# Performance work log

Measured on AMD Instinct MI355X. Metric: run time of the kernel, lower is better.

## Reference

```python
import jax, jax.numpy as jnp
import numpy as np

N = 20000
F_IN = 500
HID = 64
CLS = 16
H = 4
K_KNN = 10
NEG_SLOPE = 0.2


def _edges(key, n_rand):
    # random edges plus self-loops (mirrors add_self_loops in the torch code)
    src = jax.random.randint(key, (n_rand,), 0, N)
    dst = jax.random.randint(jax.random.fold_in(key, 1), (n_rand,), 0, N)
    loops = jnp.arange(N)
    return jnp.stack([jnp.concatenate([src, loops]), jnp.concatenate([dst, loops])]).astype(jnp.int32)


def setup_inputs():
    key = jax.random.key(0)
    ks = jax.random.split(key, 40)
    inp = {}
    inp['x'] = jax.random.normal(ks[0], (N, F_IN), jnp.float32)
    inp['edge_index_1'] = _edges(ks[1], 16 * N)          # 1-hop graph, 340k edges
    inp['edge_index_2'] = _edges(ks[2], 32 * N)          # denser 2-hop graph, 660k edges
    knn_src = jnp.repeat(jnp.arange(N), K_KNN)
    knn_dst = jax.random.randint(ks[3], (K_KNN * N,), 0, N)
    inp['edge_index_knn'] = jnp.stack([knn_src, knn_dst]).astype(jnp.int32)

    def p(k, shape):
        return jax.random.normal(k, shape, jnp.float32) * 0.05

    dims = {1: (F_IN, HID), 2: (HID, CLS), 3: (F_IN, HID), 4: (HID, CLS), 5: (F_IN, HID), 6: (HID, CLS)}
    i = 4
    for j in range(1, 7):
        fi, fo = dims[j]
        inp[f'W{j}'] = p(ks[i], (fi, H, fo)); i += 1
        inp[f'as{j}'] = p(ks[i], (H, fo)); i += 1
        inp[f'ad{j}'] = p(ks[i], (H, fo)); i += 1
        inp[f'b{j}'] = jnp.zeros((fo,), jnp.float32)
    for j in range(1, 4):
        inp[f'lin{j}_w'] = p(ks[i], (CLS, CLS)); i += 1
        inp[f'lin{j}_b'] = jnp.zeros((CLS,), jnp.float32)
    inp['agg_w'] = p(ks[i], (CLS,))
    return inp


def gat_conv(x, ei, W, a_s, a_d, b):
    # PyG GATConv, concat=False (mean over heads). W: [F,H,D], a_s/a_d: [H,D], b: [D]
    src, dst = ei[0], ei[1]
    z = jnp.einsum('nf,fhd->nhd', x, W)                 # [N,H,D]
    e_src = jnp.sum(z * a_s, -1)                         # [N,H]
    e_dst = jnp.sum(z * a_d, -1)                         # [N,H]
    e = jax.nn.leaky_relu(e_src[src] + e_dst[dst], NEG_SLOPE)   # [E,H]
    m = jax.ops.segment_max(e, dst, num_segments=N)      # per-dst softmax (edge softmax)
    p = jnp.exp(e - m[dst])
    s = jax.ops.segment_sum(p, dst, num_segments=N)
    alpha = p / (s[dst] + 1e-16)                         # [E,H]
    out = jax.ops.segment_sum(alpha[:, :, None] * z[src], dst, num_segments=N)  # [N,H,D]
    return out.mean(1) + b


def reference(x, edge_index_1, edge_index_2, edge_index_knn,
              W1, as1, ad1, b1, W2, as2, ad2, b2,
              W3, as3, ad3, b3, W4, as4, ad4, b4,
              W5, as5, ad5, b5, W6, as6, ad6, b6,
              lin1_w, lin1_b, lin2_w, lin2_b, lin3_w, lin3_b, agg_w):
    # eval mode: dropout is a no-op
    h1 = jax.nn.relu(gat_conv(x, edge_index_1, W1, as1, ad1, b1))
    h1 = gat_conv(h1, edge_index_1, W2, as2, ad2, b2)
    h2 = jax.nn.relu(gat_conv(x, edge_index_2, W3, as3, ad3, b3))
    h2 = gat_conv(h2, edge_index_2, W4, as4, ad4, b4)
    h3 = jax.nn.relu(gat_conv(x, edge_index_knn, W5, as5, ad5, b5))
    h3 = gat_conv(h3, edge_index_knn, W6, as6, ad6, b6)

    a1 = jnp.tanh(h1 @ lin1_w + lin1_b) @ agg_w          # [N]
    a2 = jnp.tanh(h2 @ lin2_w + lin2_b) @ agg_w
    a3 = jnp.tanh(h3 @ lin3_w + lin3_b) @ agg_w
    a = jax.nn.softmax(jnp.stack([a1, a2, a3], axis=1), axis=1)  # [N,3]
    h = a[:, 0:1] * h1 + a[:, 1:2] * h2 + a[:, 2:3] * h3
    return jax.nn.log_softmax(h, axis=1)
```

## Files before the change

### kernel.cpp

```cpp
#include <hip/hip_runtime.h>
#include <hip/hip_bf16.h>
#include <math.h>

#define N_NODES 20000
#define MP      20096
#define FIN     500
#define KP      512
#define NBUCK   157

typedef unsigned short u16;
typedef unsigned char  u8;
typedef __attribute__((ext_vector_type(8))) short   short8;
typedef __attribute__((ext_vector_type(2))) unsigned uv2;
typedef __attribute__((ext_vector_type(4))) unsigned uv4;
typedef __attribute__((ext_vector_type(2))) float   f32x2;
typedef __attribute__((ext_vector_type(4))) float   f32x4;

__device__ __forceinline__ float b2f(u16 u){
  union { unsigned int i; float f; } v; v.i = ((unsigned int)u) << 16; return v.f;
}
__device__ __forceinline__ u16 f2b(float f){
  __hip_bfloat16 h = __float2bfloat16(f);
  return *reinterpret_cast<u16*>(&h);
}
__device__ __forceinline__ float lrelu(float x){ return x >= 0.f ? x : 0.2f * x; }
__device__ __forceinline__ float ldp(const void* p, int i, int bf){
  return bf ? b2f(((const u16*)p)[i]) : ((const float*)p)[i];
}
__device__ __forceinline__ u8 f2fp8(float f){
  return (u8)(__builtin_amdgcn_cvt_pk_fp8_f32(f, 0.f, 0, false) & 0xff);
}
template<bool HI>
__device__ __forceinline__ f32x2 fp8pair(unsigned w){
  return __builtin_amdgcn_cvt_pk_f32_fp8((int)w, HI);
}
__device__ __forceinline__ void gll16(const u16* g, u16* l){
  __builtin_amdgcn_global_load_lds(
      (const __attribute__((address_space(1))) unsigned int*)g,
      (__attribute__((address_space(3))) unsigned int*)l, 16, 0, 0);
}
__device__ __forceinline__ void barrier_lgkm(){
  asm volatile("s_waitcnt lgkmcnt(0)" ::: "memory");
  __builtin_amdgcn_s_barrier();
  asm volatile("" ::: "memory");
}
__device__ __forceinline__ float ftanh(float x){
  float ex = __expf(2.f * x);
  return 1.f - 2.f / (ex + 1.f);
}

__global__ __launch_bounds__(1024) void detect_dtype_kernel(const unsigned int* __restrict__ xw, int nwords,
                                                            int* __restrict__ flag){
  __shared__ int cnt;
  if (threadIdx.x == 0) cnt = 0;
  __syncthreads();
  int c = 0;
  for (int i = threadIdx.x; i < nwords; i += 1024){
    unsigned e = (xw[i] >> 7) & 0xFF;
    if (e >= 0x70 && e <= 0x8F) c++;
  }
  atomicAdd(&cnt, c);
  __syncthreads();
  if (threadIdx.x == 0) *flag = (cnt * 2 > nwords) ? 1 : 0;
}

#define CHA 8192
#define PB  1024
__global__ __launch_bounds__(PB) void prep_kernel(
    const void* __restrict__ x, u16* __restrict__ xp,
    const void* Wb0, const void* Wb1, const void* Wb2,
    const void* Ws0, const void* Ws1, const void* Ws2,
    u16* ob0, u16* ob1, u16* ob2, u16* os0, u16* os1, u16* os2,
    const int* s0, const int* s1, const int* s2,
    const int* d0, const int* d1, const int* d2,
    int E0, int E1, int E2, int S0, int S1, int S2, int EB,
    int* __restrict__ bucketCur, unsigned* p0, unsigned* p1, unsigned* p2,
    const int* __restrict__ flag){
  __shared__ int hb[NBUCK];
  __shared__ int loff[NBUCK];
  __shared__ int hbase[NBUCK];
  __shared__ unsigned shp[CHA];
  __shared__ u8 shb[CHA];
  __shared__ u16 tile[64][65];
  int bf = *flag;
  int tid = threadIdx.x;
  if (blockIdx.y == 0){
    int t = blockIdx.x * PB + tid;
    if (t >= MP * 64) return;
    int row = t >> 6;
    int j0  = (t & 63) * 8;
    short8 v = {0,0,0,0,0,0,0,0};
    if (row < N_NODES){
      if (j0 + 8 <= FIN){
        if (bf){
          const ushort4* xr = (const ushort4*)((const u16*)x + (size_t)row * FIN + j0);
          ushort4 a = xr[0], b = xr[1];
          v[0]=(short)a.x; v[1]=(short)a.y; v[2]=(short)a.z; v[3]=(short)a.w;
          v[4]=(short)b.x; v[5]=(short)b.y; v[6]=(short)b.z; v[7]=(short)b.w;
        } else {
          const float4* xr = (const float4*)((const float*)x + (size_t)row * FIN + j0);
          float4 a = xr[0], b = xr[1];
          v[0]=(short)f2b(a.x); v[1]=(short)f2b(a.y); v[2]=(short)f2b(a.z); v[3]=(short)f2b(a.w);
          v[4]=(short)f2b(b.x); v[5]=(short)f2b(b.y); v[6]=(short)f2b(b.z); v[7]=(short)f2b(b.w);
        }
      } else {
#pragma unroll
        for (int j = 0; j < 8; ++j){
          int k = j0 + j;
          u16 val = 0;
          if (k < FIN)
            val = bf ? ((const u16*)x)[(size_t)row * FIN + k]
                     : f2b(((const float*)x)[(size_t)row * FIN + k]);
          v[j] = (short)val;
        }
      }
    }
    *(short8*)(xp + (size_t)row * KP + j0) = v;
  } else if (blockIdx.y == 1){
    int xb = blockIdx.x;
    if (xb >= 96 + 3) return;
    int tx = tid & 63, tyb = tid >> 6;
    const void* Wsrc; u16* O; int SRCW, SRCH, DSTW, kt, nt;
    if (xb < 96){
      int which = xb >> 5, tl = xb & 31;
      nt = (tl & 3) << 6; kt = (tl >> 2) << 6;
      Wsrc = which == 0 ? Wb0 : (which == 1 ? Wb1 : Wb2);
      O    = which == 0 ? ob0 : (which == 1 ? ob1 : ob2);
      SRCW = 256; SRCH = FIN; DSTW = KP;
    } else {
      int which = xb - 96;
      nt = 0; kt = 0;
      Wsrc = which == 0 ? Ws0 : (which == 1 ? Ws1 : Ws2);
      O    = which == 0 ? os0 : (which == 1 ? os1 : os2);
      SRCW = 64; SRCH = 64; DSTW = 64;
    }
#pragma unroll
    for (int r = 0; r < 4; ++r){
      int kl = tyb + r * 16;
      int k = kt + kl, n = nt + tx;
      u16 vv = 0;
      if (k < SRCH)
        vv = bf ? ((const u16*)Wsrc)[(size_t)k * SRCW + n]
                : f2b(((const float*)Wsrc)[(size_t)k * SRCW + n]);
      tile[kl][tx] = vv;
    }
    __syncthreads();
#pragma unroll
    for (int r = 0; r < 4; ++r){
      int nl = tyb + r * 16;
      O[(size_t)(nt + nl) * DSTW + kt + tx] = tile[tx][nl];
    }
  } else {
    int sblk = blockIdx.x;
    if (sblk >= 3 * EB) return;
    int g = sblk / EB;
    const int* src = g == 0 ? s0 : (g == 1 ? s1 : s2);
    const int* dst = g == 0 ? d0 : (g == 1 ? d1 : d2);
    unsigned* pairs = g == 0 ? p0 : (g == 1 ? p1 : p2);
    int E = g == 0 ? E0 : (g == 1 ? E1 : E2);
    int S = g == 0 ? S0 : (g == 1 ? S1 : S2);
    int base = (sblk % EB) * CHA;
    if (base >= E) return;
    if (tid < NBUCK) hb[tid] = 0;
    __syncthreads();
    constexpr int EPT = CHA / PB;
    int rk[EPT]; unsigned pr[EPT]; int bk[EPT]; bool vl[EPT];
#pragma unroll
    for (int i = 0; i < EPT; ++i){
      int e = base + i * PB + tid;
      vl[i] = e < E;
      bk[i] = 0; rk[i] = 0; pr[i] = 0;
      if (vl[i]){
        int dd = dst[e], ss = src[e];
        bk[i] = dd >> 7;
        pr[i] = ((unsigned)ss << 7) | (unsigned)(dd & 127);
        rk[i] = atomicAdd(&hb[bk[i]], 1);
      }
    }
    __syncthreads();
    int ret = 0;
    if (tid < NBUCK) ret = atomicAdd(&bucketCur[g * NBUCK + tid], hb[tid]);
    if (tid == 0){
      int run = 0;
      for (int k = 0; k < NBUCK; ++k){ loff[k] = run; run += hb[k]; }
    }
    barrier_lgkm();
#pragma unroll
    for (int i = 0; i < EPT; ++i)
      if (vl[i]){
        int j = loff[bk[i]] + rk[i];
        shp[j] = pr[i];
        shb[j] = (u8)bk[i];
      }
    if (tid < NBUCK) hbase[tid] = ret;
    __syncthreads();
    int nb = E - base; if (nb > CHA) nb = CHA;
    for (int j = tid; j < nb; j += PB){
      int b = shb[j];
      int pos = hbase[b] + (j - loff[b]);
      if (pos < S)
        pairs[(size_t)b * S + pos] = shp[j];
    }
  }
}

__global__ __launch_bounds__(1024) void csr_finalize_kernel(
    const unsigned* p0, const unsigned* p1, const unsigned* p2,
    int S0, int S1, int S2,
    const int* __restrict__ bucketCur,
    int* e0, int* e1, int* e2,
    int2* __restrict__ metaB){
  int g = blockIdx.y;
  const unsigned* pairs = g == 0 ? p0 : (g == 1 ? p1 : p2);
  int* esrc = g == 0 ? e0 : (g == 1 ? e1 : e2);
  int S = g == 0 ? S0 : (g == 1 ? S1 : S2);
  int2* meta = metaB + (size_t)g * MP;
  int b = blockIdx.x;
  int nb = bucketCur[g * NBUCK + b];
  if (nb > S) nb = S;
  const unsigned* pb = pairs + (size_t)b * S;
  int* eb = esrc + (size_t)b * S;
  __shared__ int cnt[128];
  __shared__ int loff[128];
  __shared__ int cur[128];
  if (threadIdx.x < 128) cnt[threadIdx.x] = 0;
  __syncthreads();
  for (int i = threadIdx.x; i < nb; i += 1024)
    atomicAdd(&cnt[pb[i] & 127], 1);
  __syncthreads();
  if (threadIdx.x == 0){
    int run = 0;
    for (int k = 0; k < 128; ++k){ loff[k] = run; run += cnt[k]; }
  }
  __syncthreads();
  if (threadIdx.x < 128){
    cur[threadIdx.x] = loff[threadIdx.x];
    int d = b * 128 + threadIdx.x;
    if (d < N_NODES){
      int2 m; m.x = b * S + loff[threadIdx.x]; m.y = cnt[threadIdx.x];
      meta[d] = m;
    }
  }
  __syncthreads();
  for (int i = threadIdx.x; i < nb; i += 1024){
    unsigned u = pb[i];
    int slot = atomicAdd(&cur[u & 127], 1);
    eb[slot] = (int)(u >> 7);
  }
}

__global__ __launch_bounds__(256) void gemm_big_kernel(const u16* __restrict__ A,
    const u16* B0, const u16* B1, const u16* B2,
    u8* C0, u8* C1, u8* C2,
    const void* as0, const void* as1, const void* as2,
    const void* ad0, const void* ad1, const void* ad2,
    float* __restrict__ esB, float* __restrict__ edB,
    const int* __restrict__ flag, int M){
  int g = blockIdx.z;
  const u16* BT = g == 0 ? B0 : (g == 1 ? B1 : B2);
  u8* C = g == 0 ? C0 : (g == 1 ? C1 : C2);
  const void* as_ = g == 0 ? as0 : (g == 1 ? as1 : as2);
  const void* ad_ = g == 0 ? ad0 : (g == 1 ? ad1 : ad2);
  float* es = esB + (size_t)g * N_NODES * 4;
  float* ed = edB + (size_t)g * N_NODES * 4;
  __shared__ alignas(16) u16 As[128 * 64];
  __shared__ alignas(16) u16 Bs[128 * 64];
  const int K = KP, Nn = 256;
  int t = threadIdx.x, lane = t & 63, w = t >> 6;
  int m0 = blockIdx.y * 128, n0 = blockIdx.x * 128;
  int mw = (w >> 1) * 64, nw = (w & 1) * 64;
  f32x4 acc[4][4] = {};
  for (int k0 = 0; k0 < K; k0 += 64){
    __syncthreads();
#pragma unroll
    for (int i = 0; i < 4; ++i){
      int c = i * 256 + w * 64 + lane;
      int row = c >> 3, slot = c & 7;
      int kk = ((slot ^ (row & 7))) * 8;
      gll16(A  + (size_t)(m0 + row) * K + k0 + kk, As + (size_t)(i * 256 + w * 64) * 8);
      gll16(BT + (size_t)(n0 + row) * K + k0 + kk, Bs + (size_t)(i * 256 + w * 64) * 8);
    }
    __syncthreads();
#pragma unroll
    for (int ks = 0; ks < 2; ++ks){
      short8 af[4], bfr[4];
#pragma unroll
      for (int mi = 0; mi < 4; ++mi){
        int row = mw + mi * 16 + (lane & 15);
        int sl = (ks * 4 + (lane >> 4)) ^ (row & 7);
        af[mi] = *(const short8*)(As + (size_t)row * 64 + sl * 8);
      }
#pragma unroll
      for (int ni = 0; ni < 4; ++ni){
        int row = nw + ni * 16 + (lane & 15);
        int sl = (ks * 4 + (lane >> 4)) ^ (row & 7);
        bfr[ni] = *(const short8*)(Bs + (size_t)row * 64 + sl * 8);
      }
#pragma unroll
      for (int mi = 0; mi < 4; ++mi)
#pragma unroll
        for (int ni = 0; ni < 4; ++ni)
          acc[mi][ni] = __builtin_amdgcn_mfma_f32_16x16x32_bf16(af[mi], bfr[ni], acc[mi][ni], 0, 0, 0);
    }
  }
  int bf = *flag;
#pragma unroll
  for (int mi = 0; mi < 4; ++mi)
#pragma unroll
    for (int ni = 0; ni < 4; ++ni)
#pragma unroll
      for (int r = 0; r < 4; ++r){
        int row = m0 + mw + mi * 16 + (lane >> 4) * 4 + r;
        int col = n0 + nw + ni * 16 + (lane & 15);
        if (row < M) C[(size_t)row * Nn + col] = f2fp8(acc[mi][ni][r]);
      }
  {
    int h = (n0 + nw) >> 6;
    float asv[4], adv[4];
#pragma unroll
    for (int ni = 0; ni < 4; ++ni){
      int col = n0 + nw + ni * 16 + (lane & 15);
      asv[ni] = ldp(as_, col, bf);
      adv[ni] = ldp(ad_, col, bf);
    }
#pragma unroll
    for (int mi = 0; mi < 4; ++mi)
#pragma unroll
      for (int r = 0; r < 4; ++r){
        float ps = 0.f, pd2 = 0.f;
#pragma unroll
        for (int ni = 0; ni < 4; ++ni){
          ps  += acc[mi][ni][r] * asv[ni];
          pd2 += acc[mi][ni][r] * adv[ni];
        }
#pragma unroll
        for (int m2 = 1; m2 < 16; m2 <<= 1){
          ps  += __shfl_xor(ps, m2);
          pd2 += __shfl_xor(pd2, m2);
        }
        int row = m0 + mw + mi * 16 + (lane >> 4) * 4 + r;
        if ((lane & 15) == 0 && row < M){
          es[(size_t)row * 4 + h] = ps;
          ed[(size_t)row * 4 + h] = pd2;
        }
      }
  }
}

__global__ __launch_bounds__(256) void gemm_small_kernel(
    const u16* A0, const u16* A1, const u16* A2,
    const u16* B0, const u16* B1, const u16* B2,
    u8* C0, u8* C1, u8* C2,
    const void* as0, const void* as1, const void* as2,
    const void* ad0, const void* ad1, const void* ad2,
    float* __restrict__ esB, float* __restrict__ edB,
    const int* __restrict__ flag, int M){
  int g = blockIdx.y;
  const u16* A  = g == 0 ? A0 : (g == 1 ? A1 : A2);
  const u16* BT = g == 0 ? B0 : (g == 1 ? B1 : B2);
  u8* C = g == 0 ? C0 : (g == 1 ? C1 : C2);
  const void* as_ = g == 0 ? as0 : (g == 1 ? as1 : as2);
  const void* ad_ = g == 0 ? ad0 : (g == 1 ? ad1 : ad2);
  float* es = esB + (size_t)g * N_NODES * 4;
  float* ed = edB + (size_t)g * N_NODES * 4;
  __shared__ alignas(16) u16 As[64 * 64];
  __shared__ alignas(16) u16 Bs[64 * 64];
  int t = threadIdx.x, lane = t & 63, w = t >> 6;
  int m0 = blockIdx.x * 64;
#pragma unroll
  for (int i = 0; i < 2; ++i){
    int c = i * 256 + w * 64 + lane;
    int row = c >> 3, slot = c & 7;
    int kk = ((slot ^ (row & 7))) * 8;
    gll16(A  + (size_t)(m0 + row) * 64 + kk, As + (size_t)(i * 256 + w * 64) * 8);
    gll16(BT + (size_t)row * 64 + kk,        Bs + (size_t)(i * 256 + w * 64) * 8);
  }
  __syncthreads();
  f32x4 acc[4] = {};
  int mw = w * 16;
#pragma unroll
  for (int ks = 0; ks < 2; ++ks){
    int rowa = mw + (lane & 15);
    int sla = (ks * 4 + (lane >> 4)) ^ (rowa & 7);
    short8 af = *(const short8*)(As + (size_t)rowa * 64 + sla * 8);
#pragma unroll
    for (int ni = 0; ni < 4; ++ni){
      int rowb = ni * 16 + (lane & 15);
      int slb = (ks * 4 + (lane >> 4)) ^ (rowb & 7);
      short8 bv = *(const short8*)(Bs + (size_t)rowb * 64 + slb * 8);
      acc[ni] = __builtin_amdgcn_mfma_f32_16x16x32_bf16(af, bv, acc[ni], 0, 0, 0);
    }
  }
  int bf = *flag;
#pragma unroll
  for (int ni = 0; ni < 4; ++ni)
#pragma unroll
    for (int r = 0; r < 4; ++r){
      int row = m0 + mw + (lane >> 4) * 4 + r;
      int col = ni * 16 + (lane & 15);
      if (row < M) C[(size_t)row * 64 + col] = f2fp8(acc[ni][r]);
    }
  {
    float asv[4], adv[4];
#pragma unroll
    for (int ni = 0; ni < 4; ++ni){
      int col = ni * 16 + (lane & 15);
      asv[ni] = ldp(as_, col, bf);
      adv[ni] = ldp(ad_, col, bf);
    }
#pragma unroll
    for (int r = 0; r < 4; ++r){
      float ps[4], pd2[4];
#pragma unroll
      for (int ni = 0; ni < 4; ++ni){ ps[ni] = acc[ni][r] * asv[ni]; pd2[ni] = acc[ni][r] * adv[ni]; }
#pragma unroll
      for (int m2 = 1; m2 < 16; m2 <<= 1)
#pragma unroll
        for (int ni = 0; ni < 4; ++ni){
          ps[ni]  += __shfl_xor(ps[ni], m2);
          pd2[ni] += __shfl_xor(pd2[ni], m2);
        }
      int row = m0 + mw + (lane >> 4) * 4 + r;
      if ((lane & 15) == 0 && row < M){
#pragma unroll
        for (int ni = 0; ni < 4; ++ni){
          es[(size_t)row * 4 + ni] = ps[ni];
          ed[(size_t)row * 4 + ni] = pd2[ni];
        }
      }
    }
  }
}

template<int DT, bool RELU, bool BF16OUT, int PIPE, int VB>
__global__ __launch_bounds__(256) void gat_agg5_kernel(
    const u8* z0, const u8* z1, const u8* z2,
    const float* __restrict__ esB, const float* __restrict__ edB,
    const int2* __restrict__ metaB,
    const int* e0p, const int* e1p, const int* e2p,
    const void* b0, const void* b1, const void* b2,
    void* o0, void* o1, void* o2,
    const int* __restrict__ flag){
  int g = blockIdx.y;
  const u8* z = g == 0 ? z0 : (g == 1 ? z1 : z2);
  const int* esrc = g == 0 ? e0p : (g == 1 ? e1p : e2p);
  const void* bias = g == 0 ? b0 : (g == 1 ? b1 : b2);
  void* out = g == 0 ? o0 : (g == 1 ? o1 : o2);
  const float* es = esB + (size_t)g * N_NODES * 4;
  const float* ed = edB + (size_t)g * N_NODES * 4;
  const int2* meta = metaB + (size_t)g * MP;
  int bf = *flag;

  int d = (blockIdx.x * 256 + threadIdx.x) >> 6;
  int lane = threadIdx.x & 63;
  if (d >= N_NODES) return;
  constexpr int LPG = DT / VB;
  constexpr int G   = 64 / LPG;
  constexpr int HD  = DT / 4;
  constexpr int NW  = VB / 4;
  int grp = lane / LPG;
  int li  = lane % LPG;
  int c0  = li * VB;
  int h   = c0 / HD;

  int2 md = meta[d];
  int deg = md.y;
  const int* ep = esrc + md.x;
  float edh = ed[(unsigned)d * 4 + h];

  f32x2 acc2[VB / 2];
#pragma unroll
  for (int k = 0; k < VB / 2; ++k) acc2[k] = f32x2{0.f, 0.f};
  float sacc = 0.f;

  int steps = (deg + PIPE * G - 1) / (PIPE * G);
  for (int tb = 0; tb < steps; ++tb){
    int e0 = tb * PIPE * G + grp;
    int s[PIPE]; float q[PIPE]; unsigned w[PIPE][NW]; bool val[PIPE];
#pragma unroll
    for (int i = 0; i < PIPE; ++i){
      int e = e0 + i * G;
      val[i] = e < deg;
      int sl = ep[e];
      s[i] = val[i] ? sl : 0;
    }
#pragma unroll
    for (int i = 0; i < PIPE; ++i) q[i] = es[(unsigned)s[i] * 4 + h];
#pragma unroll
    for (int i = 0; i < PIPE; ++i){
      if constexpr (VB == 8){
        uv2 v = *(const uv2*)(z + (unsigned)s[i] * DT + c0);
        w[i][0] = v[0]; w[i][1] = v[1];
      } else {
        uv4 v = *(const uv4*)(z + (unsigned)s[i] * DT + c0);
        w[i][0] = v[0]; w[i][1] = v[1]; w[i][2] = v[2]; w[i][3] = v[3];
      }
    }
#pragma unroll
    for (int i = 0; i < PIPE; ++i){
      float p = val[i] ? __expf(lrelu(q[i] + edh)) : 0.f;
      sacc += p;
      f32x2 p2 = { p, p };
#pragma unroll
      for (int k = 0; k < NW; ++k){
        f32x2 lo = fp8pair<false>(w[i][k]);
        f32x2 hi = fp8pair<true >(w[i][k]);
        acc2[2 * k]     = __builtin_elementwise_fma(p2, lo, acc2[2 * k]);
        acc2[2 * k + 1] = __builtin_elementwise_fma(p2, hi, acc2[2 * k + 1]);
      }
    }
  }

#pragma unroll
  for (int m = LPG; m < 64; m <<= 1){
    sacc += __shfl_xor(sacc, m);
#pragma unroll
    for (int k = 0; k < VB / 2; ++k){
      acc2[k][0] += __shfl_xor(acc2[k][0], m);
      acc2[k][1] += __shfl_xor(acc2[k][1], m);
    }
  }
  float inv = 1.f / (sacc + 1e-16f);
  float v8[VB];
#pragma unroll
  for (int j = 0; j < VB; ++j) v8[j] = acc2[j / 2][j & 1] * inv;
#pragma unroll
  for (int m = HD / VB; m < LPG; m <<= 1)
#pragma unroll
    for (int j = 0; j < VB; ++j) v8[j] += __shfl_xor(v8[j], m);

  if (lane < HD / VB){
    if constexpr (BF16OUT){
#pragma unroll
      for (int b = 0; b < VB / 8; ++b){
        short8 ov;
#pragma unroll
        for (int j = 0; j < 8; ++j){
          float o = v8[b * 8 + j] * 0.25f + ldp(bias, c0 + b * 8 + j, bf);
          if (RELU) o = fmaxf(o, 0.f);
          ov[j] = (short)f2b(o);
        }
        *(short8*)((u16*)out + (size_t)d * HD + c0 + b * 8) = ov;
      }
    } else {
      float* op = (float*)out + (size_t)d * HD + c0;
#pragma unroll
      for (int b = 0; b < VB / 4; ++b){
        float o[4];
#pragma unroll
        for (int j = 0; j < 4; ++j){
          o[j] = v8[b * 4 + j] * 0.25f + ldp(bias, c0 + b * 4 + j, bf);
          if (RELU) o[j] = fmaxf(o[j], 0.f);
        }
        *(float4*)(op + b * 4) = make_float4(o[0], o[1], o[2], o[3]);
      }
    }
  }
}

__global__ __launch_bounds__(256) void final_combine_kernel(
    const float* __restrict__ h1, const float* __restrict__ h2, const float* __restrict__ h3,
    const void* l1w, const void* l1b, const void* l2w, const void* l2b,
    const void* l3w, const void* l3b, const void* aggw,
    void* __restrict__ outv, int n, const int* __restrict__ flag){
  __shared__ float Lw[3][16][16];
  __shared__ float Lb[3][16];
  __shared__ float Ag[16];
  int t = threadIdx.x;
  int bf = *flag;
  {
    const void* ws[3] = { l1w, l2w, l3w };
    for (int g = 0; g < 3; ++g) Lw[g][t / 16][t % 16] = ldp(ws[g], t, bf);
    if (t < 16){
      Lb[0][t] = ldp(l1b, t, bf); Lb[1][t] = ldp(l2b, t, bf); Lb[2][t] = ldp(l3b, t, bf);
      Ag[t] = ldp(aggw, t, bf);
    }
  }
  __syncthreads();
  int node = blockIdx.x * 256 + t;
  if (node >= n) return;
  const float* hp[3] = { h1, h2, h3 };
  float hv[3][16];
  float a[3];
  for (int g = 0; g < 3; ++g){
    const float4* h4 = (const float4*)(hp[g] + (size_t)node * 16);
#pragma unroll
    for (int q = 0; q < 4; ++q){
      float4 f = h4[q];
      hv[g][q * 4 + 0] = f.x; hv[g][q * 4 + 1] = f.y;
      hv[g][q * 4 + 2] = f.z; hv[g][q * 4 + 3] = f.w;
    }
    float dot = 0.f;
#pragma unroll
    for (int j = 0; j < 16; ++j){
      float acc2 = Lb[g][j];
#pragma unroll
      for (int i = 0; i < 16; ++i) acc2 += hv[g][i] * Lw[g][i][j];
      dot += ftanh(acc2) * Ag[j];
    }
    a[g] = dot;
  }
  float am = fmaxf(a[0], fmaxf(a[1], a[2]));
  float e0 = __expf(a[0] - am), e1 = __expf(a[1] - am), e2 = __expf(a[2] - am);
  float einv = 1.f / (e0 + e1 + e2);
  float w0 = e0 * einv, w1 = e1 * einv, w2 = e2 * einv;
  float hh[16];
  float hmax = -INFINITY;
#pragma unroll
  for (int i = 0; i < 16; ++i){
    hh[i] = w0 * hv[0][i] + w1 * hv[1][i] + w2 * hv[2][i];
    hmax = fmaxf(hmax, hh[i]);
  }
  float se = 0.f;
#pragma unroll
  for (int i = 0; i < 16; ++i) se += __expf(hh[i] - hmax);
  float ls = hmax + logf(se);
#pragma unroll
  for (int i = 0; i < 16; ++i){
    float o = hh[i] - ls;
    if (bf) ((__hip_bfloat16*)outv)[(size_t)node * 16 + i] = __float2bfloat16(o);
    else    ((float*)outv)[(size_t)node * 16 + i] = o;
  }
}

extern "C" void kernel_launch(void* const* d_in, const int* in_sizes, int n_in,
                              void* d_out, int out_size, void* d_ws, size_t ws_size,
                              hipStream_t stream){
  const void* x = d_in[0];
  const int* ei[3] = { (const int*)d_in[1], (const int*)d_in[2], (const int*)d_in[3] };
  int E[3] = { in_sizes[1] / 2, in_sizes[2] / 2, in_sizes[3] / 2 };
  int Emax = E[0] > E[1] ? E[0] : E[1]; if (E[2] > Emax) Emax = E[2];
  int EB = (Emax + CHA - 1) / CHA;
  int S[3];
  for (int g = 0; g < 3; ++g){
    long s = ((long)E[g] * 27 / 20) / NBUCK + 64;
    s &= ~63L; if (s > 8192) s = 8192;
    S[g] = (int)s;
  }
  const void *W[6], *as_[6], *ad_[6], *bb[6];
  for (int j = 0; j < 6; ++j){
    W[j]   = d_in[4 + 4 * j];
    as_[j] = d_in[5 + 4 * j];
    ad_[j] = d_in[6 + 4 * j];
    bb[j]  = d_in[7 + 4 * j];
  }
  const void* l1w = d_in[28]; const void* l1b = d_in[29];
  const void* l2w = d_in[30]; const void* l2b = d_in[31];
  const void* l3w = d_in[32]; const void* l3b = d_in[33];
  const void* agg = d_in[34];

  char* p = (char*)d_ws;
  auto alloc = [&](size_t bytes) -> void* {
    void* r = (void*)p;
    p += (bytes + 255) & ~(size_t)255;
    return r;
  };
  int* dflag = (int*)alloc(256);
  u16* xp = (u16*)alloc((size_t)MP * KP * 2);
  u16* hmid[3]; for (int g = 0; g < 3; ++g) hmid[g] = xp + (size_t)g * MP * 64;
  u16* wtb[3]; for (int g = 0; g < 3; ++g) wtb[g] = (u16*)alloc((size_t)256 * KP * 2);
  u16* wts[3]; for (int g = 0; g < 3; ++g) wts[g] = (u16*)alloc((size_t)64 * 64 * 2);
  u8* zf[3];   for (int g = 0; g < 3; ++g) zf[g]  = (u8*)alloc((size_t)N_NODES * 256 + 256);
  float* hbr[3]; for (int g = 0; g < 3; ++g) hbr[g] = (float*)alloc((size_t)N_NODES * 16 * 4);
  float* esB = (float*)alloc((size_t)3 * N_NODES * 4 * 4);
  float* edB = (float*)alloc((size_t)3 * N_NODES * 4 * 4);
  int* bucketCur = (int*)alloc((size_t)3 * NBUCK * 4);
  int2* metaB    = (int2*)alloc((size_t)3 * MP * 8);
  int* esrc[3];
  for (int g = 0; g < 3; ++g) esrc[g] = (int*)alloc(((size_t)NBUCK * S[g] + 256) * 4);
  unsigned* pairs[3];
  for (int g = 0; g < 3; ++g) pairs[g] = (unsigned*)alloc(((size_t)NBUCK * S[g] + 256) * 4);

  const int* s0 = ei[0];          const int* s1 = ei[1];          const int* s2 = ei[2];
  const int* d0 = ei[0] + E[0];   const int* d1 = ei[1] + E[1];   const int* d2 = ei[2] + E[2];

  (void)hipMemsetAsync(bucketCur, 0, (size_t)3 * NBUCK * 4, stream);
  detect_dtype_kernel<<<1, 1024, 0, stream>>>((const unsigned int*)x, 4096, dflag);
  prep_kernel<<<dim3((MP * 64 + PB - 1) / PB, 3), PB, 0, stream>>>(
      x, xp, W[0], W[2], W[4], W[1], W[3], W[5],
      wtb[0], wtb[1], wtb[2], wts[0], wts[1], wts[2],
      s0, s1, s2, d0, d1, d2, E[0], E[1], E[2], S[0], S[1], S[2], EB,
      bucketCur, pairs[0], pairs[1], pairs[2], dflag);
  csr_finalize_kernel<<<dim3(NBUCK, 3), 1024, 0, stream>>>(
      pairs[0], pairs[1], pairs[2], S[0], S[1], S[2], bucketCur,
      esrc[0], esrc[1], esrc[2], metaB);

  const int convGrid = (N_NODES + 3) / 4;

  gemm_big_kernel<<<dim3(2, MP / 128, 3), 256, 0, stream>>>(
      xp, wtb[0], wtb[1], wtb[2], zf[0], zf[1], zf[2],
      as_[0], as_[2], as_[4], ad_[0], ad_[2], ad_[4], esB, edB, dflag, N_NODES);
  gat_agg5_kernel<256, true, true, 4, 16><<<dim3(convGrid, 3), 256, 0, stream>>>(
      zf[0], zf[1], zf[2], esB, edB, metaB, esrc[0], esrc[1], esrc[2],
      bb[0], bb[2], bb[4], (void*)hmid[0], (void*)hmid[1], (void*)hmid[2], dflag);

  gemm_small_kernel<<<dim3(MP / 64, 3), 256, 0, stream>>>(
      hmid[0], hmid[1], hmid[2], wts[0], wts[1], wts[2], zf[0], zf[1], zf[2],
      as_[1], as_[3], as_[5], ad_[1], ad_[3], ad_[5], esB, edB, dflag, N_NODES);
  gat_agg5_kernel<64, false, false, 4, 8><<<dim3(convGrid, 3), 256, 0, stream>>>(
      zf[0], zf[1], zf[2], esB, edB, metaB, esrc[0], esrc[1], esrc[2],
      bb[1], bb[3], bb[5], (void*)hbr[0], (void*)hbr[1], (void*)hbr[2], dflag);

  final_combine_kernel<<<(N_NODES + 255) / 256, 256, 0, stream>>>(
      hbr[0], hbr[1], hbr[2], l1w, l1b, l2w, l2b, l3w, l3b, agg,
      d_out, N_NODES, dflag);
}
```

Baseline: 329.0 us.

## Software-pipeline GAT aggregation gathers with double-buffered edge chunks

```diff
diff --git a/kernel.cpp b/kernel.cpp
--- a/kernel.cpp
+++ b/kernel.cpp
@@ -33,6 +33,9 @@
 template<bool HI>
 __device__ __forceinline__ f32x2 fp8pair(unsigned w){
   return __builtin_amdgcn_cvt_pk_f32_fp8((int)w, HI);
+}
+__device__ __forceinline__ void pkfma(f32x2& a, f32x2 p, f32x2 v){
+  asm("v_pk_fma_f32 %0, %1, %2, %0" : "+v"(a) : "v"(p), "v"(v));
 }
 __device__ __forceinline__ void gll16(const u16* g, u16* l){
   __builtin_amdgcn_global_load_lds(
@@ -458,6 +461,7 @@
   constexpr int G   = 64 / LPG;
   constexpr int HD  = DT / 4;
   constexpr int NW  = VB / 4;
+  constexpr int CHK = PIPE * G;
   int grp = lane / LPG;
   int li  = lane % LPG;
   int c0  = li * VB;
@@ -466,6 +470,8 @@
   int2 md = meta[d];
   int deg = md.y;
   const int* ep = esrc + md.x;
+  const float* esh = es + h;
+  const u8*    zl  = z + c0;
   float edh = ed[(unsigned)d * 4 + h];
 
   f32x2 acc2[VB / 2];
@@ -473,9 +479,54 @@
   for (int k = 0; k < VB / 2; ++k) acc2[k] = f32x2{0.f, 0.f};
   float sacc = 0.f;
 
-  int steps = (deg + PIPE * G - 1) / (PIPE * G);
-  for (int tb = 0; tb < steps; ++tb){
-    int e0 = tb * PIPE * G + grp;
+#define LOADS_(S, T) do{ int eb_ = (T) * CHK + grp; \
+  _Pragma("unroll") for (int i_ = 0; i_ < PIPE; ++i_) S[i_] = ep[eb_ + i_ * G]; }while(0)
+
+#define GATHER_(Q, W, S) do{ \
+  _Pragma("unroll") for (int i_ = 0; i_ < PIPE; ++i_) Q[i_] = esh[(unsigned)S[i_] * 4u]; \
+  _Pragma("unroll") for (int i_ = 0; i_ < PIPE; ++i_){ \
+    if constexpr (VB == 8){ uv2 v_ = *(const uv2*)(zl + (unsigned)S[i_] * DT); \
+      W[i_][0] = v_[0]; W[i_][1] = v_[1]; } \
+    else { uv4 v_ = *(const uv4*)(zl + (unsigned)S[i_] * DT); \
+      W[i_][0] = v_[0]; W[i_][1] = v_[1]; W[i_][2] = v_[2]; W[i_][3] = v_[3]; } } }while(0)
+
+#define COMPUTE_U_(Q, W) do{ \
+  _Pragma("unroll") for (int i_ = 0; i_ < PIPE; ++i_){ \
+    float p_ = __expf(lrelu(Q[i_] + edh)); \
+    sacc += p_; \
+    f32x2 p2_ = { p_, p_ }; \
+    _Pragma("unroll") for (int k_ = 0; k_ < NW; ++k_){ \
+      pkfma(acc2[2 * k_],     p2_, fp8pair<false>(W[i_][k_])); \
+      pkfma(acc2[2 * k_ + 1], p2_, fp8pair<true >(W[i_][k_])); } } }while(0)
+
+  int full = deg / CHK;
+  int rem  = deg - full * CHK;
+
+  if (full > 0){
+    int sA[PIPE], sB[PIPE];
+    float qA[PIPE], qB[PIPE];
+    unsigned wA[PIPE][NW], wB[PIPE][NW];
+    LOADS_(sA, 0);
+    GATHER_(qA, wA, sA);
+    if (full > 1) LOADS_(sB, 1);
+    int t = 0;
+    while (true){
+      if (t + 1 < full){
+        GATHER_(qB, wB, sB);
+        if (t + 2 < full) LOADS_(sA, t + 2);
+      }
+      COMPUTE_U_(qA, wA);
+      ++t; if (t >= full) break;
+      if (t + 1 < full){
+        GATHER_(qA, wA, sA);
+        if (t + 2 < full) LOADS_(sB, t + 2);
+      }
+      COMPUTE_U_(qB, wB);
+      ++t; if (t >= full) break;
+    }
+  }
+  if (rem > 0){
+    int e0 = full * CHK + grp;
     int s[PIPE]; float q[PIPE]; unsigned w[PIPE][NW]; bool val[PIPE];
 #pragma unroll
     for (int i = 0; i < PIPE; ++i){
@@ -485,14 +536,14 @@
       s[i] = val[i] ? sl : 0;
     }
 #pragma unroll
-    for (int i = 0; i < PIPE; ++i) q[i] = es[(unsigned)s[i] * 4 + h];
+    for (int i = 0; i < PIPE; ++i) q[i] = esh[(unsigned)s[i] * 4u];
 #pragma unroll
     for (int i = 0; i < PIPE; ++i){
       if constexpr (VB == 8){
-        uv2 v = *(const uv2*)(z + (unsigned)s[i] * DT + c0);
+        uv2 v = *(const uv2*)(zl + (unsigned)s[i] * DT);
         w[i][0] = v[0]; w[i][1] = v[1];
       } else {
-        uv4 v = *(const uv4*)(z + (unsigned)s[i] * DT + c0);
+        uv4 v = *(const uv4*)(zl + (unsigned)s[i] * DT);
         w[i][0] = v[0]; w[i][1] = v[1]; w[i][2] = v[2]; w[i][3] = v[3];
       }
     }
@@ -503,13 +554,14 @@
       f32x2 p2 = { p, p };
 #pragma unroll
       for (int k = 0; k < NW; ++k){
-        f32x2 lo = fp8pair<false>(w[i][k]);
-        f32x2 hi = fp8pair<true >(w[i][k]);
-        acc2[2 * k]     = __builtin_elementwise_fma(p2, lo, acc2[2 * k]);
-        acc2[2 * k + 1] = __builtin_elementwise_fma(p2, hi, acc2[2 * k + 1]);
-      }
-    }
-  }
+        pkfma(acc2[2 * k],     p2, fp8pair<false>(w[i][k]));
+        pkfma(acc2[2 * k + 1], p2, fp8pair<true >(w[i][k]));
+      }
+    }
+  }
+#undef LOADS_
+#undef GATHER_
+#undef COMPUTE_U_
 
 #pragma unroll
   for (int m = LPG; m < 64; m <<= 1){
@@ -697,7 +749,7 @@
   gemm_small_kernel<<<dim3(MP / 64, 3), 256, 0, stream>>>(
       hmid[0], hmid[1], hmid[2], wts[0], wts[1], wts[2], zf[0], zf[1], zf[2],
       as_[1], as_[3], as_[5], ad_[1], ad_[3], ad_[5], esB, edB, dflag, N_NODES);
-  gat_agg5_kernel<64, false, false, 4, 8><<<dim3(convGrid, 3), 256, 0, stream>>>(
+  gat_agg5_kernel<64, false, false, 2, 8><<<dim3(convGrid, 3), 256, 0, stream>>>(
       zf[0], zf[1], zf[2], esB, edB, metaB, esrc[0], esrc[1], esrc[2],
       bb[1], bb[3], bb[5], (void*)hbr[0], (void*)hbr[1], (void*)hbr[2], dflag);
 
```

New measurement: 345.2 us. 4.9% more time.

## Remap aggregation blocks per XCD for L2 locality, retune pipeline, force packed FMA

Applied to the files above, without the earlier changes.

```diff
diff --git a/kernel.cpp b/kernel.cpp
--- a/kernel.cpp
+++ b/kernel.cpp
@@ -7,6 +7,10 @@
 #define FIN     500
 #define KP      512
 #define NBUCK   157
+#define BPG     5000
+#define NXCD    8
+#define CPX     1875
+#define CPGX    625
 
 typedef unsigned short u16;
 typedef unsigned char  u8;
@@ -33,6 +37,9 @@
 template<bool HI>
 __device__ __forceinline__ f32x2 fp8pair(unsigned w){
   return __builtin_amdgcn_cvt_pk_f32_fp8((int)w, HI);
+}
+__device__ __forceinline__ void pkfma(f32x2& a, f32x2 p, f32x2 v){
+  asm("v_pk_fma_f32 %0, %1, %2, %0" : "+v"(a) : "v"(p), "v"(v));
 }
 __device__ __forceinline__ void gll16(const u16* g, u16* l){
   __builtin_amdgcn_global_load_lds(
@@ -441,7 +448,11 @@
     const void* b0, const void* b1, const void* b2,
     void* o0, void* o1, void* o2,
     const int* __restrict__ flag){
-  int g = blockIdx.y;
+  int bx = blockIdx.x;
+  int xcd = bx & (NXCD - 1);
+  int j   = bx >> 3;
+  int g   = j / CPGX;
+  int blk = xcd * CPGX + (j - g * CPGX);
   const u8* z = g == 0 ? z0 : (g == 1 ? z1 : z2);
   const int* esrc = g == 0 ? e0p : (g == 1 ? e1p : e2p);
   const void* bias = g == 0 ? b0 : (g == 1 ? b1 : b2);
@@ -451,7 +462,7 @@
   const int2* meta = metaB + (size_t)g * MP;
   int bf = *flag;
 
-  int d = (blockIdx.x * 256 + threadIdx.x) >> 6;
+  int d = blk * 4 + (threadIdx.x >> 6);
   int lane = threadIdx.x & 63;
   if (d >= N_NODES) return;
   constexpr int LPG = DT / VB;
@@ -503,10 +514,8 @@
       f32x2 p2 = { p, p };
 #pragma unroll
       for (int k = 0; k < NW; ++k){
-        f32x2 lo = fp8pair<false>(w[i][k]);
-        f32x2 hi = fp8pair<true >(w[i][k]);
-        acc2[2 * k]     = __builtin_elementwise_fma(p2, lo, acc2[2 * k]);
-        acc2[2 * k + 1] = __builtin_elementwise_fma(p2, hi, acc2[2 * k + 1]);
+        pkfma(acc2[2 * k],     p2, fp8pair<false>(w[i][k]));
+        pkfma(acc2[2 * k + 1], p2, fp8pair<true >(w[i][k]));
       }
     }
   }
@@ -523,11 +532,11 @@
   float inv = 1.f / (sacc + 1e-16f);
   float v8[VB];
 #pragma unroll
-  for (int j = 0; j < VB; ++j) v8[j] = acc2[j / 2][j & 1] * inv;
+  for (int j2 = 0; j2 < VB; ++j2) v8[j2] = acc2[j2 / 2][j2 & 1] * inv;
 #pragma unroll
   for (int m = HD / VB; m < LPG; m <<= 1)
 #pragma unroll
-    for (int j = 0; j < VB; ++j) v8[j] += __shfl_xor(v8[j], m);
+    for (int j2 = 0; j2 < VB; ++j2) v8[j2] += __shfl_xor(v8[j2], m);
 
   if (lane < HD / VB){
     if constexpr (BF16OUT){
@@ -535,10 +544,10 @@
       for (int b = 0; b < VB / 8; ++b){
         short8 ov;
 #pragma unroll
-        for (int j = 0; j < 8; ++j){
-          float o = v8[b * 8 + j] * 0.25f + ldp(bias, c0 + b * 8 + j, bf);
+        for (int j2 = 0; j2 < 8; ++j2){
+          float o = v8[b * 8 + j2] * 0.25f + ldp(bias, c0 + b * 8 + j2, bf);
           if (RELU) o = fmaxf(o, 0.f);
-          ov[j] = (short)f2b(o);
+          ov[j2] = (short)f2b(o);
         }
         *(short8*)((u16*)out + (size_t)d * HD + c0 + b * 8) = ov;
       }
@@ -548,9 +557,9 @@
       for (int b = 0; b < VB / 4; ++b){
         float o[4];
 #pragma unroll
-        for (int j = 0; j < 4; ++j){
-          o[j] = v8[b * 4 + j] * 0.25f + ldp(bias, c0 + b * 4 + j, bf);
-          if (RELU) o[j] = fmaxf(o[j], 0.f);
+        for (int j2 = 0; j2 < 4; ++j2){
+          o[j2] = v8[b * 4 + j2] * 0.25f + ldp(bias, c0 + b * 4 + j2, bf);
+          if (RELU) o[j2] = fmaxf(o[j2], 0.f);
         }
         *(float4*)(op + b * 4) = make_float4(o[0], o[1], o[2], o[3]);
       }
@@ -685,19 +694,17 @@
       pairs[0], pairs[1], pairs[2], S[0], S[1], S[2], bucketCur,
       esrc[0], esrc[1], esrc[2], metaB);
 
-  const int convGrid = (N_NODES + 3) / 4;
-
   gemm_big_kernel<<<dim3(2, MP / 128, 3), 256, 0, stream>>>(
       xp, wtb[0], wtb[1], wtb[2], zf[0], zf[1], zf[2],
       as_[0], as_[2], as_[4], ad_[0], ad_[2], ad_[4], esB, edB, dflag, N_NODES);
-  gat_agg5_kernel<256, true, true, 4, 16><<<dim3(convGrid, 3), 256, 0, stream>>>(
+  gat_agg5_kernel<256, true, true, 6, 8><<<dim3(3 * BPG), 256, 0, stream>>>(
       zf[0], zf[1], zf[2], esB, edB, metaB, esrc[0], esrc[1], esrc[2],
       bb[0], bb[2], bb[4], (void*)hmid[0], (void*)hmid[1], (void*)hmid[2], dflag);
 
   gemm_small_kernel<<<dim3(MP / 64, 3), 256, 0, stream>>>(
       hmid[0], hmid[1], hmid[2], wts[0], wts[1], wts[2], zf[0], zf[1], zf[2],
       as_[1], as_[3], as_[5], ad_[1], ad_[3], ad_[5], esB, edB, dflag, N_NODES);
-  gat_agg5_kernel<64, false, false, 4, 8><<<dim3(convGrid, 3), 256, 0, stream>>>(
+  gat_agg5_kernel<64, false, false, 4, 8><<<dim3(3 * BPG), 256, 0, stream>>>(
       zf[0], zf[1], zf[2], esB, edB, metaB, esrc[0], esrc[1], esrc[2],
       bb[1], bb[3], bb[5], (void*)hbr[0], (void*)hbr[1], (void*)hbr[2], dflag);
 
```

After: 328.2 us. No clear change (-0.2%).
